# Optimization experiments

Hardware: AMD Instinct MI355X
Metric: run time of the kernel (lower is better)

## Reference

```python
import jax, jax.numpy as jnp
import numpy as np

N_NODES = 100000
N_EDGES = 1200000
D_IN = 64
D_OUT = 32
BN_EPS = 1e-5


def setup_inputs() -> dict:
    key = jax.random.key(0)
    ks = jax.random.split(key, 8)
    x = jax.random.normal(ks[0], (N_NODES, D_IN), dtype=jnp.float32)
    edge_index = jax.random.randint(ks[1], (2, N_EDGES), 0, N_NODES, dtype=jnp.int64)
    W1s = jax.random.normal(ks[2], (3, D_IN, D_IN), dtype=jnp.float32) * 0.05
    b1s = jax.random.normal(ks[3], (3, D_IN), dtype=jnp.float32) * 0.05
    W2s = jax.random.normal(ks[4], (3, D_IN, D_IN), dtype=jnp.float32) * 0.05
    b2s = jax.random.normal(ks[5], (3, D_IN), dtype=jnp.float32) * 0.05
    gammas = jnp.ones((3, D_IN), dtype=jnp.float32)
    betas = jnp.zeros((3, D_IN), dtype=jnp.float32)
    epss = jnp.zeros((3,), dtype=jnp.float32)  # GINConv train_eps init value 0
    lin_w = jax.random.normal(ks[6], (D_IN, D_OUT), dtype=jnp.float32) * 0.05
    lin_b = jnp.zeros((D_OUT,), dtype=jnp.float32)
    return {"x": x, "edge_index": edge_index, "W1s": W1s, "b1s": b1s,
            "W2s": W2s, "b2s": b2s, "gammas": gammas, "betas": betas,
            "epss": epss, "lin_w": lin_w, "lin_b": lin_b}


def reference(x, edge_index, W1s, b1s, W2s, b2s, gammas, betas, epss, lin_w, lin_b):
    # PyG GINConv (source_to_target): out_i = nn((1+eps)*x_i + sum_{j->i} x_j)
    src = edge_index[0]
    dst = edge_index[1]
    n = x.shape[0]
    h = x
    for i in range(3):
        agg = jax.ops.segment_sum(h[src], dst, num_segments=n)  # [N, d]
        z = (1.0 + epss[i]) * h + agg
        z = jax.nn.relu(z @ W1s[i] + b1s[i])
        z = jax.nn.relu(z @ W2s[i] + b2s[i])
        # BatchNorm1d, training mode (batch statistics, biased variance)
        mu = jnp.mean(z, axis=0)
        var = jnp.var(z, axis=0)
        z = gammas[i] * (z - mu) * jax.lax.rsqrt(var + BN_EPS) + betas[i]
        h = jax.nn.relu(z)  # F.relu after each conv
    return h @ lin_w + lin_b  # [N, D_OUT]
```

## Files before the change

### kernel.cpp

```cpp
#include <hip/hip_runtime.h>
#include <hip/hip_fp16.h>

#define NBMAX 256
#define CHB   7168

typedef _Float16 half8 __attribute__((ext_vector_type(8)));
typedef float f32x4 __attribute__((ext_vector_type(4)));

__device__ __forceinline__ unsigned short f2h(float f) {
    __half h = __float2half_rn(f);
    return *(unsigned short*)&h;
}

__device__ __forceinline__ int scan256(int v, int* wsum, int* woff) {
    int t = threadIdx.x, lane = t & 63, wv = t >> 6;
    int x = v;
    #pragma unroll
    for (int d = 1; d < 64; d <<= 1) {
        int y = __shfl_up(x, d, 64);
        if (lane >= d) x += y;
    }
    if (lane == 63) wsum[wv] = x;
    __syncthreads();
    if (t == 0) {
        int a = 0;
        #pragma unroll
        for (int i = 0; i < 4; ++i) { woff[i] = a; a += wsum[i]; }
    }
    __syncthreads();
    return x - v + woff[wv];
}

__global__ __launch_bounds__(256) void gin_init(const void* __restrict__ edge,
                                                int* __restrict__ flag,
                                                int* __restrict__ cbcnt, int nb,
                                                float* __restrict__ stats, int E) {
    int t = threadIdx.x;
    for (int i = t; i < nb; i += 256) cbcnt[i] = 0;
    for (int i = t; i < 384; i += 256) stats[i] = 0.f;
    if (t == 0) {
        const int* p = (const int*)edge;
        int is64 = 1;
        int m = (E < 64) ? E : 64;
        for (int i = 0; i < m; ++i)
            if (p[2 * i + 1] != 0) is64 = 0;
        *flag = is64;
    }
}

__global__ __launch_bounds__(256) void gin_x16(const float* __restrict__ x,
                                               unsigned short* __restrict__ o, int n16) {
    int i = blockIdx.x * 256 + threadIdx.x;
    if (i >= n16) return;
    float4 v = ((const float4*)x)[i];
    ushort4 u;
    u.x = f2h(v.x); u.y = f2h(v.y); u.z = f2h(v.z); u.w = f2h(v.w);
    ((ushort4*)o)[i] = u;
}

__global__ __launch_bounds__(256) void gin_cbhist(const void* __restrict__ edge,
                                                  const int* __restrict__ flag,
                                                  int* __restrict__ cbcnt, int E, int nb) {
    __shared__ int lc[NBMAX];
    int t = threadIdx.x;
    if (t < nb) lc[t] = 0;
    __syncthreads();
    int is64 = *flag;
    int stride = gridDim.x * 256;
    for (int e = blockIdx.x * 256 + t; e < E; e += stride) {
        int d = is64 ? (int)((const long long*)edge)[E + e] : ((const int*)edge)[E + e];
        atomicAdd(&lc[d >> 9], 1);
    }
    __syncthreads();
    if (t < nb && lc[t]) atomicAdd(&cbcnt[t], lc[t]);
}

__global__ __launch_bounds__(256) void gin_cbscan(const int* __restrict__ cbcnt,
                                                  int* __restrict__ cbbase,
                                                  int* __restrict__ cbcursor, int nb,
                                                  int* __restrict__ rowptr, int n, int E) {
    __shared__ int wsum[4], woff[4];
    int t = threadIdx.x;
    int v = (t < nb) ? cbcnt[t] : 0;
    int excl = scan256(v, wsum, woff);
    if (t < nb) { cbbase[t] = excl; cbcursor[t] = excl; }
    if (t == nb - 1) cbbase[nb] = excl + v;
    if (t == 0) rowptr[n] = E;
}

__global__ __launch_bounds__(256) void gin_binscatter(const void* __restrict__ edge,
                                                      const int* __restrict__ flag,
                                                      int* __restrict__ cbcursor,
                                                      uint2* __restrict__ ebuf, int E, int nb) {
    __shared__ int cnt[NBMAX];
    __shared__ int dlt[NBMAX];
    __shared__ int cur[NBMAX];
    __shared__ int wsum[4], woff[4];
    __shared__ uint2 buf[CHB];
    int t = threadIdx.x;
    int beg = blockIdx.x * CHB;
    int m = E - beg; if (m > CHB) m = CHB;
    if (t < nb) cnt[t] = 0;
    __syncthreads();
    int is64 = *flag;
    for (int j = t; j < m; j += 256) {
        int e = beg + j;
        int d = is64 ? (int)((const long long*)edge)[E + e] : ((const int*)edge)[E + e];
        atomicAdd(&cnt[d >> 9], 1);
    }
    __syncthreads();
    int v = (t < nb) ? cnt[t] : 0;
    int excl = scan256(v, wsum, woff);
    if (t < nb) {
        int gb = v ? atomicAdd(&cbcursor[t], v) : 0;
        dlt[t] = gb - excl;
        cur[t] = excl;
    }
    __syncthreads();
    for (int j = t; j < m; j += 256) {
        int e = beg + j;
        int s, d;
        if (is64) {
            s = (int)((const long long*)edge)[e];
            d = (int)((const long long*)edge)[E + e];
        } else {
            s = ((const int*)edge)[e];
            d = ((const int*)edge)[E + e];
        }
        int p = atomicAdd(&cur[d >> 9], 1);
        buf[p] = make_uint2((unsigned)s, (unsigned)d);
    }
    __syncthreads();
    for (int j = t; j < m; j += 256) {
        uint2 ed = buf[j];
        ebuf[j + dlt[(int)(ed.y >> 9)]] = ed;
    }
}

__global__ __launch_bounds__(256) void gin_build(const uint2* __restrict__ ebuf,
                                                 const int* __restrict__ cbbase,
                                                 int* __restrict__ rowptr,
                                                 int* __restrict__ col, int n) {
    __shared__ int cnt[512];
    __shared__ int off[512];
    __shared__ int wsum[4], woff[4];
    int b = blockIdx.x, t = threadIdx.x;
    int beg = cbbase[b], end = cbbase[b + 1];
    cnt[t] = 0; cnt[t + 256] = 0;
    __syncthreads();
    for (int j = beg + t; j < end; j += 256)
        atomicAdd(&cnt[(int)(ebuf[j].y & 511)], 1);
    __syncthreads();
    int v0 = cnt[2 * t], v1 = cnt[2 * t + 1];
    int ep = scan256(v0 + v1, wsum, woff);
    off[2 * t] = ep;
    off[2 * t + 1] = ep + v0;
    __syncthreads();
    int node0 = b * 512 + 2 * t;
    if (node0 < n) rowptr[node0] = beg + off[2 * t];
    if (node0 + 1 < n) rowptr[node0 + 1] = beg + off[2 * t + 1];
    __syncthreads();
    for (int j = beg + t; j < end; j += 256) {
        uint2 ed = ebuf[j];
        int p = atomicAdd(&off[(int)(ed.y & 511)], 1);
        col[beg + p] = (int)ed.x;
    }
}

template <bool APPLY>
__device__ __forceinline__ void accum8(float* acc, uint4 u,
                                       const float* sc, const float* sh) {
    float v[8];
    float2 f;
    f = __half22float2(*(const __half2*)&u.x); v[0] = f.x; v[1] = f.y;
    f = __half22float2(*(const __half2*)&u.y); v[2] = f.x; v[3] = f.y;
    f = __half22float2(*(const __half2*)&u.z); v[4] = f.x; v[5] = f.y;
    f = __half22float2(*(const __half2*)&u.w); v[6] = f.x; v[7] = f.y;
    #pragma unroll
    for (int j = 0; j < 8; ++j)
        acc[j] += APPLY ? fmaxf(fmaf(v[j], sc[j], sh[j]), 0.f) : v[j];
}

template <bool APPLY>
__device__ __forceinline__ void gather_body(const unsigned short* __restrict__ zb,
                                            const int* __restrict__ rowptr,
                                            const int* __restrict__ col,
                                            const float* __restrict__ epss,
                                            const float* __restrict__ ss,
                                            int layer,
                                            unsigned short* __restrict__ t,
                                            int wid, int qn, int l16) {
    int r = l16 >> 3, c = l16 & 7;
    float sc[8] = {1.f, 1.f, 1.f, 1.f, 1.f, 1.f, 1.f, 1.f};
    float sh[8] = {0.f, 0.f, 0.f, 0.f, 0.f, 0.f, 0.f, 0.f};
    if (APPLY) {
        const float* p = ss + (layer - 1) * 128;
        *(float4*)&sc[0] = *(const float4*)(p + 8 * c);
        *(float4*)&sc[4] = *(const float4*)(p + 8 * c + 4);
        *(float4*)&sh[0] = *(const float4*)(p + 64 + 8 * c);
        *(float4*)&sh[4] = *(const float4*)(p + 64 + 8 * c + 4);
    }
    int r0 = rowptr[wid], r1 = rowptr[wid + 1];
    uint4 su = make_uint4(0, 0, 0, 0);
    if (r == 0) su = *(const uint4*)(zb + (size_t)wid * 64 + 8 * c);

    float acc[8] = {0.f, 0.f, 0.f, 0.f, 0.f, 0.f, 0.f, 0.f};
    for (int base = r0; base < r1; base += 16) {
        int ce = base + l16;
        int ci = col[ce < r1 ? ce : r1 - 1];
        uint4 u[8];
        bool p[8];
        #pragma unroll
        for (int s = 0; s < 8; ++s) {
            int j = 2 * s + r;
            p[s] = (base + j) < r1;
            int idx = __shfl(ci, 16 * qn + j);
            if (p[s]) u[s] = *(const uint4*)(zb + (size_t)idx * 64 + 8 * c);
        }
        #pragma unroll
        for (int s = 0; s < 8; ++s)
            if (p[s]) accum8<APPLY>(acc, u[s], sc, sh);
    }
    #pragma unroll
    for (int j = 0; j < 8; ++j)
        acc[j] += __shfl_xor(acc[j], 8);
    if (r == 0) {
        float e1 = 1.f + epss[layer];
        float s[8];
        float2 f;
        f = __half22float2(*(const __half2*)&su.x); s[0] = f.x; s[1] = f.y;
        f = __half22float2(*(const __half2*)&su.y); s[2] = f.x; s[3] = f.y;
        f = __half22float2(*(const __half2*)&su.z); s[4] = f.x; s[5] = f.y;
        f = __half22float2(*(const __half2*)&su.w); s[6] = f.x; s[7] = f.y;
        #pragma unroll
        for (int j = 0; j < 8; ++j) {
            float v = APPLY ? fmaxf(fmaf(s[j], sc[j], sh[j]), 0.f) : s[j];
            acc[j] = fmaf(e1, v, acc[j]);
        }
        uint4 o;
        o.x = (unsigned)f2h(acc[0]) | ((unsigned)f2h(acc[1]) << 16);
        o.y = (unsigned)f2h(acc[2]) | ((unsigned)f2h(acc[3]) << 16);
        o.z = (unsigned)f2h(acc[4]) | ((unsigned)f2h(acc[5]) << 16);
        o.w = (unsigned)f2h(acc[6]) | ((unsigned)f2h(acc[7]) << 16);
        *(uint4*)(t + (size_t)wid * 64 + 8 * c) = o;
    }
}

__global__ __launch_bounds__(256) void gin_gather(const unsigned short* __restrict__ zb,
                                                  const int* __restrict__ rowptr,
                                                  const int* __restrict__ col,
                                                  const float* __restrict__ epss,
                                                  const float* __restrict__ ss,
                                                  int layer, int apply,
                                                  unsigned short* __restrict__ t, int n) {
    int gw = (blockIdx.x * 256 + threadIdx.x) >> 6;
    int lane = threadIdx.x & 63;
    int qn = lane >> 4;
    int wid = gw * 4 + qn;
    int l16 = lane & 15;
    if (wid >= n) return;
    if (apply)
        gather_body<true>(zb, rowptr, col, epss, ss, layer, t, wid, qn, l16);
    else
        gather_body<false>(zb, rowptr, col, epss, ss, layer, t, wid, qn, l16);
}

__global__ __launch_bounds__(256) void gin_mlp(const unsigned short* __restrict__ t_in,
                                               unsigned short* __restrict__ z16,
                                               const float* __restrict__ W1g,
                                               const float* __restrict__ b1g,
                                               const float* __restrict__ W2g,
                                               const float* __restrict__ b2g,
                                               float* __restrict__ stats, int layer, int n) {
    __shared__ _Float16 Wt[2 * 64 * 72];
    __shared__ _Float16 Z1[128 * 72];
    __shared__ float sS[64], sQ[64];
    int tid = threadIdx.x;
    int base = blockIdx.x * 128;
    const float* __restrict__ W1 = W1g + layer * 4096;
    const float* __restrict__ W2 = W2g + layer * 4096;

    for (int i = tid; i < 4096; i += 256) {
        int k = i >> 6, nn = i & 63;
        Wt[nn * 72 + k]        = (_Float16)W1[i];
        Wt[4608 + nn * 72 + k] = (_Float16)W2[i];
    }
    if (tid < 64) { sS[tid] = 0.f; sQ[tid] = 0.f; }
    __syncthreads();

    int lane = tid & 63, wv = tid >> 6;
    int g = lane >> 4, q = lane & 15;
    int n0 = 32 * wv + q;
    int n1 = n0 + 16;

    const _Float16* tp = (const _Float16*)t_in + (size_t)base * 64;
    half8 tb00 = *(const half8*)(tp + (size_t)n0 * 64 + 8 * g);
    half8 tb01 = *(const half8*)(tp + (size_t)n0 * 64 + 32 + 8 * g);
    half8 tb10 = *(const half8*)(tp + (size_t)n1 * 64 + 8 * g);
    half8 tb11 = *(const half8*)(tp + (size_t)n1 * 64 + 32 + 8 * g);

    f32x4 acc[2][4];
    #pragma unroll
    for (int nt = 0; nt < 2; ++nt)
        #pragma unroll
        for (int ft = 0; ft < 4; ++ft)
            acc[nt][ft] = (f32x4){0.f, 0.f, 0.f, 0.f};

    #pragma unroll
    for (int ft = 0; ft < 4; ++ft) {
        half8 a0 = *(const half8*)&Wt[(16 * ft + q) * 72 + 8 * g];
        half8 a1 = *(const half8*)&Wt[(16 * ft + q) * 72 + 32 + 8 * g];
        acc[0][ft] = __builtin_amdgcn_mfma_f32_16x16x32_f16(a0, tb00, acc[0][ft], 0, 0, 0);
        acc[0][ft] = __builtin_amdgcn_mfma_f32_16x16x32_f16(a1, tb01, acc[0][ft], 0, 0, 0);
        acc[1][ft] = __builtin_amdgcn_mfma_f32_16x16x32_f16(a0, tb10, acc[1][ft], 0, 0, 0);
        acc[1][ft] = __builtin_amdgcn_mfma_f32_16x16x32_f16(a1, tb11, acc[1][ft], 0, 0, 0);
    }

    #pragma unroll
    for (int ft = 0; ft < 4; ++ft) {
        float4 b = *(const float4*)(b1g + layer * 64 + 16 * ft + 4 * g);
        #pragma unroll
        for (int nt = 0; nt < 2; ++nt) {
            int node = nt ? n1 : n0;
            float v0 = fmaxf(acc[nt][ft][0] + b.x, 0.f);
            float v1 = fmaxf(acc[nt][ft][1] + b.y, 0.f);
            float v2 = fmaxf(acc[nt][ft][2] + b.z, 0.f);
            float v3 = fmaxf(acc[nt][ft][3] + b.w, 0.f);
            uint2 pk;
            pk.x = (unsigned)f2h(v0) | ((unsigned)f2h(v1) << 16);
            pk.y = (unsigned)f2h(v2) | ((unsigned)f2h(v3) << 16);
            *(uint2*)&Z1[node * 72 + 16 * ft + 4 * g] = pk;
        }
    }

    half8 zb00 = *(const half8*)&Z1[n0 * 72 + 8 * g];
    half8 zb01 = *(const half8*)&Z1[n0 * 72 + 32 + 8 * g];
    half8 zb10 = *(const half8*)&Z1[n1 * 72 + 8 * g];
    half8 zb11 = *(const half8*)&Z1[n1 * 72 + 32 + 8 * g];
    #pragma unroll
    for (int nt = 0; nt < 2; ++nt)
        #pragma unroll
        for (int ft = 0; ft < 4; ++ft)
            acc[nt][ft] = (f32x4){0.f, 0.f, 0.f, 0.f};
    #pragma unroll
    for (int ft = 0; ft < 4; ++ft) {
        half8 a0 = *(const half8*)&Wt[4608 + (16 * ft + q) * 72 + 8 * g];
        half8 a1 = *(const half8*)&Wt[4608 + (16 * ft + q) * 72 + 32 + 8 * g];
        acc[0][ft] = __builtin_amdgcn_mfma_f32_16x16x32_f16(a0, zb00, acc[0][ft], 0, 0, 0);
        acc[0][ft] = __builtin_amdgcn_mfma_f32_16x16x32_f16(a1, zb01, acc[0][ft], 0, 0, 0);
        acc[1][ft] = __builtin_amdgcn_mfma_f32_16x16x32_f16(a0, zb10, acc[1][ft], 0, 0, 0);
        acc[1][ft] = __builtin_amdgcn_mfma_f32_16x16x32_f16(a1, zb11, acc[1][ft], 0, 0, 0);
    }

    #pragma unroll
    for (int ft = 0; ft < 4; ++ft) {
        float4 b = *(const float4*)(b2g + layer * 64 + 16 * ft + 4 * g);
        float s[4] = {0.f, 0.f, 0.f, 0.f};
        float sq[4] = {0.f, 0.f, 0.f, 0.f};
        #pragma unroll
        for (int nt = 0; nt < 2; ++nt) {
            int node = base + (nt ? n1 : n0);
            float v0 = fmaxf(acc[nt][ft][0] + b.x, 0.f);
            float v1 = fmaxf(acc[nt][ft][1] + b.y, 0.f);
            float v2 = fmaxf(acc[nt][ft][2] + b.z, 0.f);
            float v3 = fmaxf(acc[nt][ft][3] + b.w, 0.f);
            if (node < n) {
                s[0] += v0; sq[0] += v0 * v0;
                s[1] += v1; sq[1] += v1 * v1;
                s[2] += v2; sq[2] += v2 * v2;
                s[3] += v3; sq[3] += v3 * v3;
                uint2 pk;
                pk.x = (unsigned)f2h(v0) | ((unsigned)f2h(v1) << 16);
                pk.y = (unsigned)f2h(v2) | ((unsigned)f2h(v3) << 16);
                *(uint2*)(z16 + (size_t)node * 64 + 16 * ft + 4 * g) = pk;
            }
        }
        #pragma unroll
        for (int off = 1; off < 16; off <<= 1) {
            #pragma unroll
            for (int r2 = 0; r2 < 4; ++r2) {
                s[r2] += __shfl_xor(s[r2], off);
                sq[r2] += __shfl_xor(sq[r2], off);
            }
        }
        if (q == 0) {
            #pragma unroll
            for (int r2 = 0; r2 < 4; ++r2) {
                atomicAdd(&sS[16 * ft + 4 * g + r2], s[r2]);
                atomicAdd(&sQ[16 * ft + 4 * g + r2], sq[r2]);
            }
        }
    }
    __syncthreads();
    if (tid < 64) {
        atomicAdd(&stats[layer * 128 + tid], sS[tid]);
        atomicAdd(&stats[layer * 128 + 64 + tid], sQ[tid]);
    }
}

__global__ void gin_bnfin(const float* __restrict__ stats, const float* __restrict__ gammas,
                          const float* __restrict__ betas, float* __restrict__ ss,
                          int layer, float n) {
    int f = threadIdx.x;
    float mu = stats[layer * 128 + f] / n;
    float var = stats[layer * 128 + 64 + f] / n - mu * mu;
    float rs = rsqrtf(var + 1e-5f);
    float g = gammas[layer * 64 + f];
    float b = betas[layer * 64 + f];
    ss[layer * 128 + f] = g * rs;
    ss[layer * 128 + 64 + f] = b - g * rs * mu;
}

__global__ __launch_bounds__(256) void gin_lin(const unsigned short* __restrict__ zin,
                                               const float* __restrict__ ss,
                                               const float* __restrict__ lw,
                                               const float* __restrict__ lb,
                                               float* __restrict__ out, int n) {
    __shared__ float Z[128 * 68];
    int tid = threadIdx.x;
    int base = blockIdx.x * 128;
    {
        const ushort4* __restrict__ src = (const ushort4*)(zin + (size_t)base * 64);
        #pragma unroll
        for (int it = 0; it < 8; ++it) {
            int idx4 = it * 256 + tid;
            int row = idx4 >> 4, c = (idx4 & 15) * 4;
            float4 v = make_float4(0.f, 0.f, 0.f, 0.f);
            if (base + row < n) {
                ushort4 u = src[idx4];
                float2 f0 = __half22float2(*(const __half2*)&u.x);
                float2 f1 = __half22float2(*(const __half2*)&u.z);
                v = make_float4(f0.x, f0.y, f1.x, f1.y);
            }
            float4 sc = *(const float4*)(ss + 256 + c);
            float4 sh = *(const float4*)(ss + 256 + 64 + c);
            float4 r;
            r.x = fmaxf(fmaf(v.x, sc.x, sh.x), 0.f);
            r.y = fmaxf(fmaf(v.y, sc.y, sh.y), 0.f);
            r.z = fmaxf(fmaf(v.z, sc.z, sh.z), 0.f);
            r.w = fmaxf(fmaf(v.w, sc.w, sh.w), 0.f);
            *(float4*)&Z[row * 68 + c] = r;
        }
    }
    __syncthreads();
    int tx = tid & 7, ty = tid >> 3;
    float acc[4][4];
    {
        float4 b = *(const float4*)(lb + 4 * tx);
        #pragma unroll
        for (int r = 0; r < 4; ++r) {
            acc[r][0] = b.x; acc[r][1] = b.y; acc[r][2] = b.z; acc[r][3] = b.w;
        }
    }
    #pragma unroll 4
    for (int k = 0; k < 64; ++k) {
        float4 w = *(const float4*)(lw + k * 32 + 4 * tx);
        #pragma unroll
        for (int r = 0; r < 4; ++r) {
            float a = Z[(ty + 32 * r) * 68 + k];
            acc[r][0] = fmaf(a, w.x, acc[r][0]);
            acc[r][1] = fmaf(a, w.y, acc[r][1]);
            acc[r][2] = fmaf(a, w.z, acc[r][2]);
            acc[r][3] = fmaf(a, w.w, acc[r][3]);
        }
    }
    #pragma unroll
    for (int r = 0; r < 4; ++r) {
        int row = base + ty + 32 * r;
        if (row < n) {
            float4 v;
            v.x = acc[r][0]; v.y = acc[r][1]; v.z = acc[r][2]; v.w = acc[r][3];
            *(float4*)(out + (size_t)row * 32 + 4 * tx) = v;
        }
    }
}

extern "C" void kernel_launch(void* const* d_in, const int* in_sizes, int n_in,
                              void* d_out, int out_size, void* d_ws, size_t ws_size,
                              hipStream_t stream) {
    const float* x      = (const float*)d_in[0];
    const void*  edge   = d_in[1];
    const float* W1s    = (const float*)d_in[2];
    const float* b1s    = (const float*)d_in[3];
    const float* W2s    = (const float*)d_in[4];
    const float* b2s    = (const float*)d_in[5];
    const float* gammas = (const float*)d_in[6];
    const float* betas  = (const float*)d_in[7];
    const float* epss   = (const float*)d_in[8];
    const float* lin_w  = (const float*)d_in[9];
    const float* lin_b  = (const float*)d_in[10];
    float* out = (float*)d_out;

    const int N = in_sizes[0] / 64;
    const int E = in_sizes[1] / 2;
    const int NB = (N + 511) >> 9;
    const float fN = (float)N;

    char* w = (char*)d_ws;
    auto take = [&](size_t bytes) {
        char* p = w;
        w += (bytes + 255) & ~(size_t)255;
        return p;
    };
    unsigned short* A  = (unsigned short*)take((size_t)N * 64 * 4);
    unsigned short* zb = (unsigned short*)take((size_t)N * 64 * 2);
    int*   col     = (int*)take((size_t)E * 4);
    int*   rowptr  = (int*)take((size_t)(N + 1) * 4);
    int*   cbcnt   = (int*)take((size_t)NBMAX * 4);
    int*   cbbase  = (int*)take((size_t)(NBMAX + 1) * 4);
    int*   cbcur   = (int*)take((size_t)NBMAX * 4);
    float* stats   = (float*)take(3 * 128 * 4);
    float* ss      = (float*)take(3 * 128 * 4);
    int*   flag    = (int*)take(4);
    uint2*          ebuf = (uint2*)A;
    unsigned short* x16  = zb;

    gin_init<<<1, 256, 0, stream>>>(edge, flag, cbcnt, NB, stats, E);
    gin_x16<<<(N * 16 + 255) / 256, 256, 0, stream>>>(x, x16, N * 16);
    gin_cbhist<<<256, 256, 0, stream>>>(edge, flag, cbcnt, E, NB);
    gin_cbscan<<<1, 256, 0, stream>>>(cbcnt, cbbase, cbcur, NB, rowptr, N, E);
    gin_binscatter<<<(E + CHB - 1) / CHB, 256, 0, stream>>>(edge, flag, cbcur, ebuf, E, NB);
    gin_build<<<NB, 256, 0, stream>>>(ebuf, cbbase, rowptr, col, N);

    const int gGather = (N + 15) / 16;
    const int gMlp    = (N + 127) / 128;

    for (int L = 0; L < 3; ++L) {
        const unsigned short* zin = (L == 0) ? x16 : zb;
        gin_gather<<<gGather, 256, 0, stream>>>(zin, rowptr, col, epss, ss, L,
                                                (L > 0) ? 1 : 0, A, N);
        gin_mlp<<<gMlp, 256, 0, stream>>>(A, zb, W1s, b1s, W2s, b2s, stats, L, N);
        gin_bnfin<<<1, 64, 0, stream>>>(stats, gammas, betas, ss, L, fN);
    }
    gin_lin<<<gMlp, 256, 0, stream>>>(zb, ss, lin_w, lin_b, out, N);
}
```

Baseline: 346.8 us.

## Fuse neighbor gather into MLP kernel and fold BN finalize into consumers

Merges the per-layer gather kernel with the MLP kernel, so each 128-node block aggregates neighbors straight into shared memory and runs the MFMA MLP from there. This removes the intermediate aggregated buffer's global write and read plus a launch per layer. The BN finalize kernel is removed and each consumer block recomputes scale and shift from the stats, and the binscatter chunk size is halved. The trade-off is lower gather parallelism per block (8 sequential passes per wave) and larger per-block shared memory, which may reduce occupancy for the latency-bound gather.

```diff
diff --git a/kernel.cpp b/kernel.cpp
--- a/kernel.cpp
+++ b/kernel.cpp
@@ -2,7 +2,7 @@
 #include <hip/hip_fp16.h>
 
 #define NBMAX 256
-#define CHB   7168
+#define CHB   3584
 
 typedef _Float16 half8 __attribute__((ext_vector_type(8)));
 typedef float f32x4 __attribute__((ext_vector_type(4)));
@@ -182,122 +182,118 @@
 }
 
 template <bool APPLY>
-__device__ __forceinline__ void gather_body(const unsigned short* __restrict__ zb,
-                                            const int* __restrict__ rowptr,
-                                            const int* __restrict__ col,
-                                            const float* __restrict__ epss,
-                                            const float* __restrict__ ss,
-                                            int layer,
-                                            unsigned short* __restrict__ t,
-                                            int wid, int qn, int l16) {
+__global__ __launch_bounds__(256) void gin_layer(const unsigned short* __restrict__ zin,
+                                                 unsigned short* __restrict__ zout,
+                                                 const int* __restrict__ rowptr,
+                                                 const int* __restrict__ col,
+                                                 const float* __restrict__ epss,
+                                                 float* __restrict__ stats,
+                                                 const float* __restrict__ gammas,
+                                                 const float* __restrict__ betas,
+                                                 float fN,
+                                                 const float* __restrict__ W1g,
+                                                 const float* __restrict__ b1g,
+                                                 const float* __restrict__ W2g,
+                                                 const float* __restrict__ b2g,
+                                                 int layer, int n) {
+    __shared__ _Float16 Wt[2 * 64 * 72];
+    __shared__ _Float16 TZ[128 * 72];
+    __shared__ float ssc[64], ssh[64];
+    __shared__ float sS[64], sQ[64];
+    int tid = threadIdx.x;
+    int base = blockIdx.x * 128;
+
+    for (int i = tid; i < 4096; i += 256) {
+        int k = i >> 6, nn = i & 63;
+        Wt[nn * 72 + k]        = (_Float16)W1g[layer * 4096 + i];
+        Wt[4608 + nn * 72 + k] = (_Float16)W2g[layer * 4096 + i];
+    }
+    if (tid < 64) {
+        sS[tid] = 0.f; sQ[tid] = 0.f;
+        if (APPLY) {
+            int Lp = layer - 1;
+            float mu  = stats[Lp * 128 + tid] / fN;
+            float var = stats[Lp * 128 + 64 + tid] / fN - mu * mu;
+            float g   = gammas[Lp * 64 + tid];
+            float grs = g * rsqrtf(var + 1e-5f);
+            ssc[tid] = grs;
+            ssh[tid] = betas[Lp * 64 + tid] - grs * mu;
+        }
+    }
+    __syncthreads();
+
+    int lane = tid & 63, wv = tid >> 6;
+    int qn = lane >> 4, l16 = lane & 15;
     int r = l16 >> 3, c = l16 & 7;
+
     float sc[8] = {1.f, 1.f, 1.f, 1.f, 1.f, 1.f, 1.f, 1.f};
     float sh[8] = {0.f, 0.f, 0.f, 0.f, 0.f, 0.f, 0.f, 0.f};
     if (APPLY) {
-        const float* p = ss + (layer - 1) * 128;
-        *(float4*)&sc[0] = *(const float4*)(p + 8 * c);
-        *(float4*)&sc[4] = *(const float4*)(p + 8 * c + 4);
-        *(float4*)&sh[0] = *(const float4*)(p + 64 + 8 * c);
-        *(float4*)&sh[4] = *(const float4*)(p + 64 + 8 * c + 4);
-    }
-    int r0 = rowptr[wid], r1 = rowptr[wid + 1];
-    uint4 su = make_uint4(0, 0, 0, 0);
-    if (r == 0) su = *(const uint4*)(zb + (size_t)wid * 64 + 8 * c);
-
-    float acc[8] = {0.f, 0.f, 0.f, 0.f, 0.f, 0.f, 0.f, 0.f};
-    for (int base = r0; base < r1; base += 16) {
-        int ce = base + l16;
-        int ci = col[ce < r1 ? ce : r1 - 1];
-        uint4 u[8];
-        bool p[8];
-        #pragma unroll
-        for (int s = 0; s < 8; ++s) {
-            int j = 2 * s + r;
-            p[s] = (base + j) < r1;
-            int idx = __shfl(ci, 16 * qn + j);
-            if (p[s]) u[s] = *(const uint4*)(zb + (size_t)idx * 64 + 8 * c);
-        }
-        #pragma unroll
-        for (int s = 0; s < 8; ++s)
-            if (p[s]) accum8<APPLY>(acc, u[s], sc, sh);
-    }
-    #pragma unroll
-    for (int j = 0; j < 8; ++j)
-        acc[j] += __shfl_xor(acc[j], 8);
-    if (r == 0) {
-        float e1 = 1.f + epss[layer];
-        float s[8];
-        float2 f;
-        f = __half22float2(*(const __half2*)&su.x); s[0] = f.x; s[1] = f.y;
-        f = __half22float2(*(const __half2*)&su.y); s[2] = f.x; s[3] = f.y;
-        f = __half22float2(*(const __half2*)&su.z); s[4] = f.x; s[5] = f.y;
-        f = __half22float2(*(const __half2*)&su.w); s[6] = f.x; s[7] = f.y;
-        #pragma unroll
-        for (int j = 0; j < 8; ++j) {
-            float v = APPLY ? fmaxf(fmaf(s[j], sc[j], sh[j]), 0.f) : s[j];
-            acc[j] = fmaf(e1, v, acc[j]);
-        }
-        uint4 o;
-        o.x = (unsigned)f2h(acc[0]) | ((unsigned)f2h(acc[1]) << 16);
-        o.y = (unsigned)f2h(acc[2]) | ((unsigned)f2h(acc[3]) << 16);
-        o.z = (unsigned)f2h(acc[4]) | ((unsigned)f2h(acc[5]) << 16);
-        o.w = (unsigned)f2h(acc[6]) | ((unsigned)f2h(acc[7]) << 16);
-        *(uint4*)(t + (size_t)wid * 64 + 8 * c) = o;
-    }
-}
-
-__global__ __launch_bounds__(256) void gin_gather(const unsigned short* __restrict__ zb,
-                                                  const int* __restrict__ rowptr,
-                                                  const int* __restrict__ col,
-                                                  const float* __restrict__ epss,
-                                                  const float* __restrict__ ss,
-                                                  int layer, int apply,
-                                                  unsigned short* __restrict__ t, int n) {
-    int gw = (blockIdx.x * 256 + threadIdx.x) >> 6;
-    int lane = threadIdx.x & 63;
-    int qn = lane >> 4;
-    int wid = gw * 4 + qn;
-    int l16 = lane & 15;
-    if (wid >= n) return;
-    if (apply)
-        gather_body<true>(zb, rowptr, col, epss, ss, layer, t, wid, qn, l16);
-    else
-        gather_body<false>(zb, rowptr, col, epss, ss, layer, t, wid, qn, l16);
-}
-
-__global__ __launch_bounds__(256) void gin_mlp(const unsigned short* __restrict__ t_in,
-                                               unsigned short* __restrict__ z16,
-                                               const float* __restrict__ W1g,
-                                               const float* __restrict__ b1g,
-                                               const float* __restrict__ W2g,
-                                               const float* __restrict__ b2g,
-                                               float* __restrict__ stats, int layer, int n) {
-    __shared__ _Float16 Wt[2 * 64 * 72];
-    __shared__ _Float16 Z1[128 * 72];
-    __shared__ float sS[64], sQ[64];
-    int tid = threadIdx.x;
-    int base = blockIdx.x * 128;
-    const float* __restrict__ W1 = W1g + layer * 4096;
-    const float* __restrict__ W2 = W2g + layer * 4096;
-
-    for (int i = tid; i < 4096; i += 256) {
-        int k = i >> 6, nn = i & 63;
-        Wt[nn * 72 + k]        = (_Float16)W1[i];
-        Wt[4608 + nn * 72 + k] = (_Float16)W2[i];
-    }
-    if (tid < 64) { sS[tid] = 0.f; sQ[tid] = 0.f; }
-    __syncthreads();
-
-    int lane = tid & 63, wv = tid >> 6;
-    int g = lane >> 4, q = lane & 15;
-    int n0 = 32 * wv + q;
-    int n1 = n0 + 16;
-
-    const _Float16* tp = (const _Float16*)t_in + (size_t)base * 64;
-    half8 tb00 = *(const half8*)(tp + (size_t)n0 * 64 + 8 * g);
-    half8 tb01 = *(const half8*)(tp + (size_t)n0 * 64 + 32 + 8 * g);
-    half8 tb10 = *(const half8*)(tp + (size_t)n1 * 64 + 8 * g);
-    half8 tb11 = *(const half8*)(tp + (size_t)n1 * 64 + 32 + 8 * g);
+        *(float4*)&sc[0] = *(const float4*)&ssc[8 * c];
+        *(float4*)&sc[4] = *(const float4*)&ssc[8 * c + 4];
+        *(float4*)&sh[0] = *(const float4*)&ssh[8 * c];
+        *(float4*)&sh[4] = *(const float4*)&ssh[8 * c + 4];
+    }
+    float e1 = 1.f + epss[layer];
+
+    for (int pass = 0; pass < 8; ++pass) {
+        int nl = wv * 32 + pass * 4 + qn;
+        int wid = base + nl;
+        if (wid < n) {
+            int r0 = rowptr[wid], r1 = rowptr[wid + 1];
+            uint4 su = make_uint4(0, 0, 0, 0);
+            if (r == 0) su = *(const uint4*)(zin + (size_t)wid * 64 + 8 * c);
+            float acc[8] = {0.f, 0.f, 0.f, 0.f, 0.f, 0.f, 0.f, 0.f};
+            for (int b2 = r0; b2 < r1; b2 += 16) {
+                int ce = b2 + l16;
+                int ci = col[ce < r1 ? ce : r1 - 1];
+                uint4 u[8];
+                bool p[8];
+                #pragma unroll
+                for (int s = 0; s < 8; ++s) {
+                    int j = 2 * s + r;
+                    p[s] = (b2 + j) < r1;
+                    int idx = __shfl(ci, 16 * qn + j);
+                    if (p[s]) u[s] = *(const uint4*)(zin + (size_t)idx * 64 + 8 * c);
+                }
+                #pragma unroll
+                for (int s = 0; s < 8; ++s)
+                    if (p[s]) accum8<APPLY>(acc, u[s], sc, sh);
+            }
+            #pragma unroll
+            for (int j = 0; j < 8; ++j)
+                acc[j] += __shfl_xor(acc[j], 8);
+            if (r == 0) {
+                float s[8];
+                float2 f;
+                f = __half22float2(*(const __half2*)&su.x); s[0] = f.x; s[1] = f.y;
+                f = __half22float2(*(const __half2*)&su.y); s[2] = f.x; s[3] = f.y;
+                f = __half22float2(*(const __half2*)&su.z); s[4] = f.x; s[5] = f.y;
+                f = __half22float2(*(const __half2*)&su.w); s[6] = f.x; s[7] = f.y;
+                #pragma unroll
+                for (int j = 0; j < 8; ++j) {
+                    float v = APPLY ? fmaxf(fmaf(s[j], sc[j], sh[j]), 0.f) : s[j];
+                    acc[j] = fmaf(e1, v, acc[j]);
+                }
+                uint4 o;
+                o.x = (unsigned)f2h(acc[0]) | ((unsigned)f2h(acc[1]) << 16);
+                o.y = (unsigned)f2h(acc[2]) | ((unsigned)f2h(acc[3]) << 16);
+                o.z = (unsigned)f2h(acc[4]) | ((unsigned)f2h(acc[5]) << 16);
+                o.w = (unsigned)f2h(acc[6]) | ((unsigned)f2h(acc[7]) << 16);
+                *(uint4*)&TZ[nl * 72 + 8 * c] = o;
+            }
+        } else if (r == 0) {
+            *(uint4*)&TZ[nl * 72 + 8 * c] = make_uint4(0, 0, 0, 0);
+        }
+    }
+
+    int g = qn, q = l16;
+    int n0 = 32 * wv + q, n1 = n0 + 16;
+
+    half8 tb00 = *(const half8*)&TZ[n0 * 72 + 8 * g];
+    half8 tb01 = *(const half8*)&TZ[n0 * 72 + 32 + 8 * g];
+    half8 tb10 = *(const half8*)&TZ[n1 * 72 + 8 * g];
+    half8 tb11 = *(const half8*)&TZ[n1 * 72 + 32 + 8 * g];
 
     f32x4 acc[2][4];
     #pragma unroll
@@ -329,14 +325,14 @@
             uint2 pk;
             pk.x = (unsigned)f2h(v0) | ((unsigned)f2h(v1) << 16);
             pk.y = (unsigned)f2h(v2) | ((unsigned)f2h(v3) << 16);
-            *(uint2*)&Z1[node * 72 + 16 * ft + 4 * g] = pk;
-        }
-    }
-
-    half8 zb00 = *(const half8*)&Z1[n0 * 72 + 8 * g];
-    half8 zb01 = *(const half8*)&Z1[n0 * 72 + 32 + 8 * g];
-    half8 zb10 = *(const half8*)&Z1[n1 * 72 + 8 * g];
-    half8 zb11 = *(const half8*)&Z1[n1 * 72 + 32 + 8 * g];
+            *(uint2*)&TZ[node * 72 + 16 * ft + 4 * g] = pk;
+        }
+    }
+
+    half8 zb00 = *(const half8*)&TZ[n0 * 72 + 8 * g];
+    half8 zb01 = *(const half8*)&TZ[n0 * 72 + 32 + 8 * g];
+    half8 zb10 = *(const half8*)&TZ[n1 * 72 + 8 * g];
+    half8 zb11 = *(const half8*)&TZ[n1 * 72 + 32 + 8 * g];
     #pragma unroll
     for (int nt = 0; nt < 2; ++nt)
         #pragma unroll
@@ -372,7 +368,7 @@
                 uint2 pk;
                 pk.x = (unsigned)f2h(v0) | ((unsigned)f2h(v1) << 16);
                 pk.y = (unsigned)f2h(v2) | ((unsigned)f2h(v3) << 16);
-                *(uint2*)(z16 + (size_t)node * 64 + 16 * ft + 4 * g) = pk;
+                *(uint2*)(zout + (size_t)node * 64 + 16 * ft + 4 * g) = pk;
             }
         }
         #pragma unroll
@@ -398,27 +394,34 @@
     }
 }
 
-__global__ void gin_bnfin(const float* __restrict__ stats, const float* __restrict__ gammas,
-                          const float* __restrict__ betas, float* __restrict__ ss,
-                          int layer, float n) {
-    int f = threadIdx.x;
-    float mu = stats[layer * 128 + f] / n;
-    float var = stats[layer * 128 + 64 + f] / n - mu * mu;
-    float rs = rsqrtf(var + 1e-5f);
-    float g = gammas[layer * 64 + f];
-    float b = betas[layer * 64 + f];
-    ss[layer * 128 + f] = g * rs;
-    ss[layer * 128 + 64 + f] = b - g * rs * mu;
-}
-
 __global__ __launch_bounds__(256) void gin_lin(const unsigned short* __restrict__ zin,
-                                               const float* __restrict__ ss,
+                                               const float* __restrict__ stats,
+                                               const float* __restrict__ gammas,
+                                               const float* __restrict__ betas,
+                                               float fN,
                                                const float* __restrict__ lw,
                                                const float* __restrict__ lb,
                                                float* __restrict__ out, int n) {
     __shared__ float Z[128 * 68];
     int tid = threadIdx.x;
     int base = blockIdx.x * 128;
+    int cq = (tid & 15) * 4;
+    float4 sc4, sh4;
+    {
+        float t0[4], t1[4];
+        #pragma unroll
+        for (int j = 0; j < 4; ++j) {
+            int f = cq + j;
+            float mu  = stats[256 + f] / fN;
+            float var = stats[256 + 64 + f] / fN - mu * mu;
+            float g   = gammas[128 + f];
+            float grs = g * rsqrtf(var + 1e-5f);
+            t0[j] = grs;
+            t1[j] = betas[128 + f] - grs * mu;
+        }
+        sc4 = make_float4(t0[0], t0[1], t0[2], t0[3]);
+        sh4 = make_float4(t1[0], t1[1], t1[2], t1[3]);
+    }
     {
         const ushort4* __restrict__ src = (const ushort4*)(zin + (size_t)base * 64);
         #pragma unroll
@@ -432,13 +435,11 @@
                 float2 f1 = __half22float2(*(const __half2*)&u.z);
                 v = make_float4(f0.x, f0.y, f1.x, f1.y);
             }
-            float4 sc = *(const float4*)(ss + 256 + c);
-            float4 sh = *(const float4*)(ss + 256 + 64 + c);
             float4 r;
-            r.x = fmaxf(fmaf(v.x, sc.x, sh.x), 0.f);
-            r.y = fmaxf(fmaf(v.y, sc.y, sh.y), 0.f);
-            r.z = fmaxf(fmaf(v.z, sc.z, sh.z), 0.f);
-            r.w = fmaxf(fmaf(v.w, sc.w, sh.w), 0.f);
+            r.x = fmaxf(fmaf(v.x, sc4.x, sh4.x), 0.f);
+            r.y = fmaxf(fmaf(v.y, sc4.y, sh4.y), 0.f);
+            r.z = fmaxf(fmaf(v.z, sc4.z, sh4.z), 0.f);
+            r.w = fmaxf(fmaf(v.w, sc4.w, sh4.w), 0.f);
             *(float4*)&Z[row * 68 + c] = r;
         }
     }
@@ -502,18 +503,17 @@
         w += (bytes + 255) & ~(size_t)255;
         return p;
     };
-    unsigned short* A  = (unsigned short*)take((size_t)N * 64 * 4);
-    unsigned short* zb = (unsigned short*)take((size_t)N * 64 * 2);
+    unsigned short* x16 = (unsigned short*)take((size_t)N * 64 * 2);
+    unsigned short* hA  = (unsigned short*)take((size_t)N * 64 * 2);
+    unsigned short* hB  = (unsigned short*)take((size_t)N * 64 * 2);
+    uint2* ebuf    = (uint2*)take((size_t)E * 8);
     int*   col     = (int*)take((size_t)E * 4);
     int*   rowptr  = (int*)take((size_t)(N + 1) * 4);
     int*   cbcnt   = (int*)take((size_t)NBMAX * 4);
     int*   cbbase  = (int*)take((size_t)(NBMAX + 1) * 4);
     int*   cbcur   = (int*)take((size_t)NBMAX * 4);
     float* stats   = (float*)take(3 * 128 * 4);
-    float* ss      = (float*)take(3 * 128 * 4);
     int*   flag    = (int*)take(4);
-    uint2*          ebuf = (uint2*)A;
-    unsigned short* x16  = zb;
 
     gin_init<<<1, 256, 0, stream>>>(edge, flag, cbcnt, NB, stats, E);
     gin_x16<<<(N * 16 + 255) / 256, 256, 0, stream>>>(x, x16, N * 16);
@@ -522,15 +522,16 @@
     gin_binscatter<<<(E + CHB - 1) / CHB, 256, 0, stream>>>(edge, flag, cbcur, ebuf, E, NB);
     gin_build<<<NB, 256, 0, stream>>>(ebuf, cbbase, rowptr, col, N);
 
-    const int gGather = (N + 15) / 16;
-    const int gMlp    = (N + 127) / 128;
-
-    for (int L = 0; L < 3; ++L) {
-        const unsigned short* zin = (L == 0) ? x16 : zb;
-        gin_gather<<<gGather, 256, 0, stream>>>(zin, rowptr, col, epss, ss, L,
-                                                (L > 0) ? 1 : 0, A, N);
-        gin_mlp<<<gMlp, 256, 0, stream>>>(A, zb, W1s, b1s, W2s, b2s, stats, L, N);
-        gin_bnfin<<<1, 64, 0, stream>>>(stats, gammas, betas, ss, L, fN);
-    }
-    gin_lin<<<gMlp, 256, 0, stream>>>(zb, ss, lin_w, lin_b, out, N);
-}
+    const int gMlp = (N + 127) / 128;
+
+    gin_layer<false><<<gMlp, 256, 0, stream>>>(x16, hA, rowptr, col, epss, stats,
+                                               gammas, betas, fN,
+                                               W1s, b1s, W2s, b2s, 0, N);
+    gin_layer<true><<<gMlp, 256, 0, stream>>>(hA, hB, rowptr, col, epss, stats,
+                                              gammas, betas, fN,
+                                              W1s, b1s, W2s, b2s, 1, N);
+    gin_layer<true><<<gMlp, 256, 0, stream>>>(hB, hA, rowptr, col, epss, stats,
+                                              gammas, betas, fN,
+                                              W1s, b1s, W2s, b2s, 2, N);
+    gin_lin<<<gMlp, 256, 0, stream>>>(hA, stats, gammas, betas, fN, lin_w, lin_b, out, N);
+}
```

Result: no change. 348.0 us (+0.3%).

## Use fixed-capacity dst buckets to drop the histogram and scan passes

Applied to the files above, without the earlier changes.

Each 512-node destination bucket now gets a fixed-capacity slot of BCAP entries in the edge buffer. The binscatter kernel therefore claims positions with atomics on a per-bucket counter, and the separate histogram kernel (a full pass over edge destinations) and the scan kernel are removed. CSR row pointers become separate begin and end arrays, since the buckets are no longer contiguous. The last BN finalize launch is folded into the final linear kernel, the activations are ping-ponged between two buffers, and the chunk size is halved. The cost is a larger workspace and a hard assumption that no bucket receives more than BCAP edges; skewed degree distributions would overflow a bucket.

```diff
diff --git a/kernel.cpp b/kernel.cpp
--- a/kernel.cpp
+++ b/kernel.cpp
@@ -2,7 +2,8 @@
 #include <hip/hip_fp16.h>
 
 #define NBMAX 256
-#define CHB   7168
+#define BCAP  8192
+#define CHB   3584
 
 typedef _Float16 half8 __attribute__((ext_vector_type(8)));
 typedef float f32x4 __attribute__((ext_vector_type(4)));
@@ -33,10 +34,10 @@
 
 __global__ __launch_bounds__(256) void gin_init(const void* __restrict__ edge,
                                                 int* __restrict__ flag,
-                                                int* __restrict__ cbcnt, int nb,
+                                                int* __restrict__ gcount, int nb,
                                                 float* __restrict__ stats, int E) {
     int t = threadIdx.x;
-    for (int i = t; i < nb; i += 256) cbcnt[i] = 0;
+    for (int i = t; i < nb; i += 256) gcount[i] = 0;
     for (int i = t; i < 384; i += 256) stats[i] = 0.f;
     if (t == 0) {
         const int* p = (const int*)edge;
@@ -58,39 +59,9 @@
     ((ushort4*)o)[i] = u;
 }
 
-__global__ __launch_bounds__(256) void gin_cbhist(const void* __restrict__ edge,
-                                                  const int* __restrict__ flag,
-                                                  int* __restrict__ cbcnt, int E, int nb) {
-    __shared__ int lc[NBMAX];
-    int t = threadIdx.x;
-    if (t < nb) lc[t] = 0;
-    __syncthreads();
-    int is64 = *flag;
-    int stride = gridDim.x * 256;
-    for (int e = blockIdx.x * 256 + t; e < E; e += stride) {
-        int d = is64 ? (int)((const long long*)edge)[E + e] : ((const int*)edge)[E + e];
-        atomicAdd(&lc[d >> 9], 1);
-    }
-    __syncthreads();
-    if (t < nb && lc[t]) atomicAdd(&cbcnt[t], lc[t]);
-}
-
-__global__ __launch_bounds__(256) void gin_cbscan(const int* __restrict__ cbcnt,
-                                                  int* __restrict__ cbbase,
-                                                  int* __restrict__ cbcursor, int nb,
-                                                  int* __restrict__ rowptr, int n, int E) {
-    __shared__ int wsum[4], woff[4];
-    int t = threadIdx.x;
-    int v = (t < nb) ? cbcnt[t] : 0;
-    int excl = scan256(v, wsum, woff);
-    if (t < nb) { cbbase[t] = excl; cbcursor[t] = excl; }
-    if (t == nb - 1) cbbase[nb] = excl + v;
-    if (t == 0) rowptr[n] = E;
-}
-
 __global__ __launch_bounds__(256) void gin_binscatter(const void* __restrict__ edge,
                                                       const int* __restrict__ flag,
-                                                      int* __restrict__ cbcursor,
+                                                      int* __restrict__ gcount,
                                                       uint2* __restrict__ ebuf, int E, int nb) {
     __shared__ int cnt[NBMAX];
     __shared__ int dlt[NBMAX];
@@ -112,8 +83,8 @@
     int v = (t < nb) ? cnt[t] : 0;
     int excl = scan256(v, wsum, woff);
     if (t < nb) {
-        int gb = v ? atomicAdd(&cbcursor[t], v) : 0;
-        dlt[t] = gb - excl;
+        int gb = v ? atomicAdd(&gcount[t], v) : 0;
+        dlt[t] = t * BCAP + gb - excl;
         cur[t] = excl;
     }
     __syncthreads();
@@ -138,14 +109,16 @@
 }
 
 __global__ __launch_bounds__(256) void gin_build(const uint2* __restrict__ ebuf,
-                                                 const int* __restrict__ cbbase,
-                                                 int* __restrict__ rowptr,
+                                                 const int* __restrict__ gcount,
+                                                 int* __restrict__ rowbeg,
+                                                 int* __restrict__ rowend,
                                                  int* __restrict__ col, int n) {
     __shared__ int cnt[512];
     __shared__ int off[512];
     __shared__ int wsum[4], woff[4];
     int b = blockIdx.x, t = threadIdx.x;
-    int beg = cbbase[b], end = cbbase[b + 1];
+    int beg = b * BCAP;
+    int end = beg + gcount[b];
     cnt[t] = 0; cnt[t + 256] = 0;
     __syncthreads();
     for (int j = beg + t; j < end; j += 256)
@@ -157,8 +130,14 @@
     off[2 * t + 1] = ep + v0;
     __syncthreads();
     int node0 = b * 512 + 2 * t;
-    if (node0 < n) rowptr[node0] = beg + off[2 * t];
-    if (node0 + 1 < n) rowptr[node0 + 1] = beg + off[2 * t + 1];
+    if (node0 < n) {
+        rowbeg[node0] = beg + off[2 * t];
+        rowend[node0] = beg + off[2 * t] + v0;
+    }
+    if (node0 + 1 < n) {
+        rowbeg[node0 + 1] = beg + off[2 * t + 1];
+        rowend[node0 + 1] = beg + off[2 * t + 1] + v1;
+    }
     __syncthreads();
     for (int j = beg + t; j < end; j += 256) {
         uint2 ed = ebuf[j];
@@ -183,7 +162,8 @@
 
 template <bool APPLY>
 __device__ __forceinline__ void gather_body(const unsigned short* __restrict__ zb,
-                                            const int* __restrict__ rowptr,
+                                            const int* __restrict__ rowbeg,
+                                            const int* __restrict__ rowend,
                                             const int* __restrict__ col,
                                             const float* __restrict__ epss,
                                             const float* __restrict__ ss,
@@ -200,7 +180,7 @@
         *(float4*)&sh[0] = *(const float4*)(p + 64 + 8 * c);
         *(float4*)&sh[4] = *(const float4*)(p + 64 + 8 * c + 4);
     }
-    int r0 = rowptr[wid], r1 = rowptr[wid + 1];
+    int r0 = rowbeg[wid], r1 = rowend[wid];
     uint4 su = make_uint4(0, 0, 0, 0);
     if (r == 0) su = *(const uint4*)(zb + (size_t)wid * 64 + 8 * c);
 
@@ -247,7 +227,8 @@
 }
 
 __global__ __launch_bounds__(256) void gin_gather(const unsigned short* __restrict__ zb,
-                                                  const int* __restrict__ rowptr,
+                                                  const int* __restrict__ rowbeg,
+                                                  const int* __restrict__ rowend,
                                                   const int* __restrict__ col,
                                                   const float* __restrict__ epss,
                                                   const float* __restrict__ ss,
@@ -260,9 +241,9 @@
     int l16 = lane & 15;
     if (wid >= n) return;
     if (apply)
-        gather_body<true>(zb, rowptr, col, epss, ss, layer, t, wid, qn, l16);
+        gather_body<true>(zb, rowbeg, rowend, col, epss, ss, layer, t, wid, qn, l16);
     else
-        gather_body<false>(zb, rowptr, col, epss, ss, layer, t, wid, qn, l16);
+        gather_body<false>(zb, rowbeg, rowend, col, epss, ss, layer, t, wid, qn, l16);
 }
 
 __global__ __launch_bounds__(256) void gin_mlp(const unsigned short* __restrict__ t_in,
@@ -412,13 +393,33 @@
 }
 
 __global__ __launch_bounds__(256) void gin_lin(const unsigned short* __restrict__ zin,
-                                               const float* __restrict__ ss,
+                                               const float* __restrict__ stats,
+                                               const float* __restrict__ gammas,
+                                               const float* __restrict__ betas,
+                                               float fN,
                                                const float* __restrict__ lw,
                                                const float* __restrict__ lb,
                                                float* __restrict__ out, int n) {
     __shared__ float Z[128 * 68];
     int tid = threadIdx.x;
     int base = blockIdx.x * 128;
+    int cq = (tid & 15) * 4;
+    float4 sc4, sh4;
+    {
+        float t0[4], t1[4];
+        #pragma unroll
+        for (int j = 0; j < 4; ++j) {
+            int f = cq + j;
+            float mu  = stats[256 + f] / fN;
+            float var = stats[256 + 64 + f] / fN - mu * mu;
+            float g   = gammas[128 + f];
+            float grs = g * rsqrtf(var + 1e-5f);
+            t0[j] = grs;
+            t1[j] = betas[128 + f] - grs * mu;
+        }
+        sc4 = make_float4(t0[0], t0[1], t0[2], t0[3]);
+        sh4 = make_float4(t1[0], t1[1], t1[2], t1[3]);
+    }
     {
         const ushort4* __restrict__ src = (const ushort4*)(zin + (size_t)base * 64);
         #pragma unroll
@@ -432,13 +433,11 @@
                 float2 f1 = __half22float2(*(const __half2*)&u.z);
                 v = make_float4(f0.x, f0.y, f1.x, f1.y);
             }
-            float4 sc = *(const float4*)(ss + 256 + c);
-            float4 sh = *(const float4*)(ss + 256 + 64 + c);
             float4 r;
-            r.x = fmaxf(fmaf(v.x, sc.x, sh.x), 0.f);
-            r.y = fmaxf(fmaf(v.y, sc.y, sh.y), 0.f);
-            r.z = fmaxf(fmaf(v.z, sc.z, sh.z), 0.f);
-            r.w = fmaxf(fmaf(v.w, sc.w, sh.w), 0.f);
+            r.x = fmaxf(fmaf(v.x, sc4.x, sh4.x), 0.f);
+            r.y = fmaxf(fmaf(v.y, sc4.y, sh4.y), 0.f);
+            r.z = fmaxf(fmaf(v.z, sc4.z, sh4.z), 0.f);
+            r.w = fmaxf(fmaf(v.w, sc4.w, sh4.w), 0.f);
             *(float4*)&Z[row * 68 + c] = r;
         }
     }
@@ -502,35 +501,36 @@
         w += (bytes + 255) & ~(size_t)255;
         return p;
     };
-    unsigned short* A  = (unsigned short*)take((size_t)N * 64 * 4);
-    unsigned short* zb = (unsigned short*)take((size_t)N * 64 * 2);
-    int*   col     = (int*)take((size_t)E * 4);
-    int*   rowptr  = (int*)take((size_t)(N + 1) * 4);
-    int*   cbcnt   = (int*)take((size_t)NBMAX * 4);
-    int*   cbbase  = (int*)take((size_t)(NBMAX + 1) * 4);
-    int*   cbcur   = (int*)take((size_t)NBMAX * 4);
+    unsigned short* x16 = (unsigned short*)take((size_t)N * 64 * 2);
+    unsigned short* hA  = (unsigned short*)take((size_t)N * 64 * 2);
+    unsigned short* hB  = (unsigned short*)take((size_t)N * 64 * 2);
+    unsigned short* T   = (unsigned short*)take((size_t)N * 64 * 2);
+    uint2* ebuf    = (uint2*)take((size_t)NB * BCAP * 8);
+    int*   col     = (int*)take((size_t)NB * BCAP * 4);
+    int*   rowbeg  = (int*)take((size_t)N * 4);
+    int*   rowend  = (int*)take((size_t)N * 4);
+    int*   gcount  = (int*)take((size_t)NBMAX * 4);
     float* stats   = (float*)take(3 * 128 * 4);
     float* ss      = (float*)take(3 * 128 * 4);
     int*   flag    = (int*)take(4);
-    uint2*          ebuf = (uint2*)A;
-    unsigned short* x16  = zb;
-
-    gin_init<<<1, 256, 0, stream>>>(edge, flag, cbcnt, NB, stats, E);
+
+    gin_init<<<1, 256, 0, stream>>>(edge, flag, gcount, NB, stats, E);
     gin_x16<<<(N * 16 + 255) / 256, 256, 0, stream>>>(x, x16, N * 16);
-    gin_cbhist<<<256, 256, 0, stream>>>(edge, flag, cbcnt, E, NB);
-    gin_cbscan<<<1, 256, 0, stream>>>(cbcnt, cbbase, cbcur, NB, rowptr, N, E);
-    gin_binscatter<<<(E + CHB - 1) / CHB, 256, 0, stream>>>(edge, flag, cbcur, ebuf, E, NB);
-    gin_build<<<NB, 256, 0, stream>>>(ebuf, cbbase, rowptr, col, N);
+    gin_binscatter<<<(E + CHB - 1) / CHB, 256, 0, stream>>>(edge, flag, gcount, ebuf, E, NB);
+    gin_build<<<NB, 256, 0, stream>>>(ebuf, gcount, rowbeg, rowend, col, N);
 
     const int gGather = (N + 15) / 16;
     const int gMlp    = (N + 127) / 128;
 
+    const unsigned short* zin = x16;
+    unsigned short* zout = hA;
     for (int L = 0; L < 3; ++L) {
-        const unsigned short* zin = (L == 0) ? x16 : zb;
-        gin_gather<<<gGather, 256, 0, stream>>>(zin, rowptr, col, epss, ss, L,
-                                                (L > 0) ? 1 : 0, A, N);
-        gin_mlp<<<gMlp, 256, 0, stream>>>(A, zb, W1s, b1s, W2s, b2s, stats, L, N);
-        gin_bnfin<<<1, 64, 0, stream>>>(stats, gammas, betas, ss, L, fN);
-    }
-    gin_lin<<<gMlp, 256, 0, stream>>>(zb, ss, lin_w, lin_b, out, N);
-}
+        gin_gather<<<gGather, 256, 0, stream>>>(zin, rowbeg, rowend, col, epss, ss, L,
+                                                (L > 0) ? 1 : 0, T, N);
+        gin_mlp<<<gMlp, 256, 0, stream>>>(T, zout, W1s, b1s, W2s, b2s, stats, L, N);
+        if (L < 2) gin_bnfin<<<1, 64, 0, stream>>>(stats, gammas, betas, ss, L, fN);
+        zin = zout;
+        zout = (zout == hA) ? hB : hA;
+    }
+    gin_lin<<<gMlp, 256, 0, stream>>>(zin, stats, gammas, betas, fN, lin_w, lin_b, out, N);
+}
```

New measurement: 322.8 us. 1.07x faster.
